# Kernel tuning notes

Hardware: AMD Instinct MI355X
Metric: run time of the kernel (lower is better)

The kernel has to match this reference:

```python
import jax, jax.numpy as jnp
import numpy as np

K_NN = 20  # neighbors per group (k=20 in source)


def fps_one(xyz, npoint):
    # xyz: [N,3] -> indices [npoint] via iterative furthest point sampling
    N = xyz.shape[0]
    def body(carry, _):
        dist, far = carry
        d = jnp.sum((xyz - xyz[far]) ** 2, axis=-1)
        dist = jnp.minimum(dist, d)
        return (dist, jnp.argmax(dist).astype(jnp.int32)), far
    init = (jnp.full((N,), 1e10, xyz.dtype), jnp.int32(0))
    _, idx = jax.lax.scan(body, init, None, length=npoint)
    return idx


def gather(pts, idx):
    # pts: [B,M,C], idx: [B,...] -> [B,...,C]
    return jax.vmap(lambda p, i: p[i])(pts, idx)


def knn(q, ref, k):
    # q: [B,S,3], ref: [B,M,3] -> [B,S,k] indices of nearest refs
    d = (jnp.sum(q * q, -1, keepdims=True)
         - 2.0 * jnp.einsum('bsc,bmc->bsm', q, ref)
         + jnp.sum(ref * ref, -1)[:, None, :])
    _, idx = jax.lax.top_k(-d, k)
    return idx


def sa_block(xyz, feats, npoint, W, b):
    # Set abstraction: FPS sample -> kNN group -> shared MLP -> max pool
    fidx = jax.vmap(fps_one, in_axes=(0, None))(xyz, npoint)   # [B,S]
    new_xyz = gather(xyz, fidx)                                 # [B,S,3]
    nidx = knn(new_xyz, xyz, K_NN)                              # [B,S,K]
    rel = gather(xyz, nidx) - new_xyz[:, :, None, :]            # [B,S,K,3]
    grp = jnp.concatenate([rel, gather(feats, nidx)], -1)       # [B,S,K,3+C]
    h = jax.nn.relu(jnp.einsum('bskc,cd->bskd', grp, W) + b)
    return new_xyz, jnp.max(h, axis=2)                          # [B,S,Cout]


def fp_block(xq, xr, fr, skip, W, b):
    # Feature propagation: 3-NN inverse-distance interp -> concat skip -> MLP
    idx = knn(xq, xr, 3)                                        # [B,S,3]
    d = jnp.sum((gather(xr, idx) - xq[:, :, None, :]) ** 2, -1)
    w = 1.0 / (d + 1e-8)
    w = w / jnp.sum(w, -1, keepdims=True)
    interp = jnp.einsum('bsk,bskc->bsc', w, gather(fr, idx))
    cat = jnp.concatenate([interp, skip], -1)
    return jax.nn.relu(jnp.einsum('bsc,cd->bsd', cat, W) + b)


def setup_inputs() -> dict:
    key = jax.random.key(0)
    ks = jax.random.split(key, 24)
    B, N = 8, 4096
    x = jax.random.normal(ks[0], (B, 6, N), jnp.float32)
    cls_label = jax.random.uniform(ks[1], (B, 16), jnp.float32)
    def lin(k, cin, cout):
        kw, kb = jax.random.split(k)
        s = 1.0 / np.sqrt(cin)
        return (jax.random.normal(kw, (cin, cout), jnp.float32) * s,
                jax.random.normal(kb, (cout,), jnp.float32) * 0.01)
    W0, b0 = lin(ks[2], 6, 64)
    W1, b1 = lin(ks[3], 67, 128)
    W2, b2 = lin(ks[4], 131, 256)
    W3, b3 = lin(ks[5], 259, 512)
    F3, fb3 = lin(ks[6], 768, 512)
    F2, fb2 = lin(ks[7], 640, 256)
    F1, fb1 = lin(ks[8], 320, 128)
    F0, fb0 = lin(ks[9], 150, 128)
    Wseg, bseg = lin(ks[10], 128, 50)
    return {"x": x, "cls_label": cls_label,
            "W0": W0, "b0": b0, "W1": W1, "b1": b1, "W2": W2, "b2": b2,
            "W3": W3, "b3": b3, "F3": F3, "fb3": fb3, "F2": F2, "fb2": fb2,
            "F1": F1, "fb1": fb1, "F0": F0, "fb0": fb0,
            "Wseg": Wseg, "bseg": bseg}


def reference(x, cls_label, W0, b0, W1, b1, W2, b2, W3, b3,
              F3, fb3, F2, fb2, F1, fb1, F0, fb0, Wseg, bseg):
    B, _, N = x.shape
    xyz = jnp.transpose(x[:, :3, :], (0, 2, 1))   # [B,N,3]
    nrm = jnp.transpose(x[:, 3:, :], (0, 2, 1))   # [B,N,3]
    # hierarchical set abstraction (512 -> 256 -> 128 -> 64 points)
    x1, f1 = sa_block(xyz, nrm, 512, W0, b0)      # f1: [B,512,64]
    x2, f2 = sa_block(x1, f1, 256, W1, b1)        # f2: [B,256,128]
    x3, f3 = sa_block(x2, f2, 128, W2, b2)        # f3: [B,128,256]
    x4, f4 = sa_block(x3, f3, 64, W3, b3)         # f4: [B,64,512]
    # feature propagation back up
    g3 = fp_block(x3, x4, f4, f3, F3, fb3)        # [B,128,512]
    g2 = fp_block(x2, x3, g3, f2, F2, fb2)        # [B,256,256]
    g1 = fp_block(x1, x2, g2, f1, F1, fb1)        # [B,512,128]
    cls = jnp.broadcast_to(cls_label[:, None, :], (B, N, 16))
    skip0 = jnp.concatenate([cls, xyz, nrm], -1)  # [B,N,22]
    g0 = fp_block(xyz, x1, g1, skip0, F0, fb0)    # [B,N,128]
    result = jnp.einsum('bnc,cd->bnd', g0, Wseg) + bseg  # [B,N,50]
    return result, jnp.transpose(g0, (0, 2, 1))
```

## Files before the change

### kernel.cpp

```cpp
#include <hip/hip_runtime.h>
#include <float.h>

#define B8 8
#define NPTS 4096

__global__ void split_xyz_kernel(const float* __restrict__ x,
                                 float* __restrict__ xyz, float* __restrict__ nrm,
                                 float4* __restrict__ xyz4) {
#pragma clang fp contract(off)
  int g = blockIdx.x * 256 + threadIdx.x;
  if (g >= B8 * NPTS) return;
  int b = g / NPTS, n = g % NPTS;
  const float* xb = x + (size_t)b * 6 * NPTS;
  float* o1 = xyz + (size_t)g * 3;
  float* o2 = nrm + (size_t)g * 3;
  float a0 = xb[0 * NPTS + n], a1 = xb[1 * NPTS + n], a2 = xb[2 * NPTS + n];
  o1[0] = a0; o1[1] = a1; o1[2] = a2;
  xyz4[g] = make_float4(a0, a1, a2, a0 * a0 + a1 * a1 + a2 * a2);
  o2[0] = xb[3 * NPTS + n]; o2[1] = xb[4 * NPTS + n]; o2[2] = xb[5 * NPTS + n];
}

template <int CTRL, int RM>
__device__ __forceinline__ unsigned dppmov(unsigned v) {
  return (unsigned)__builtin_amdgcn_update_dpp((int)v, (int)v, CTRL, RM, 0xf, false);
}

template <int CTRL, int RM>
__device__ __forceinline__ void red_key_max(unsigned& kh, unsigned& kl) {
  unsigned oh = dppmov<CTRL, RM>(kh);
  unsigned ol = dppmov<CTRL, RM>(kl);
  unsigned long long ko = ((unsigned long long)oh << 32) | ol;
  unsigned long long k  = ((unsigned long long)kh << 32) | kl;
  bool c = ko > k;
  kh = c ? oh : kh;
  kl = c ? ol : kl;
}

template <int CTRL, int RM>
__device__ __forceinline__ void red_key_min(unsigned& kh, unsigned& kl) {
  unsigned oh = dppmov<CTRL, RM>(kh);
  unsigned ol = dppmov<CTRL, RM>(kl);
  unsigned long long ko = ((unsigned long long)oh << 32) | ol;
  unsigned long long k  = ((unsigned long long)kh << 32) | kl;
  bool c = ko < k;
  kh = c ? oh : kh;
  kl = c ? ol : kl;
}

#define WAVE_RED_MAX(kh, kl)            \
  red_key_max<0x111, 0xf>(kh, kl);      \
  red_key_max<0x112, 0xf>(kh, kl);      \
  red_key_max<0x114, 0xf>(kh, kl);      \
  red_key_max<0x118, 0xf>(kh, kl);      \
  red_key_max<0x142, 0xa>(kh, kl);      \
  red_key_max<0x143, 0xc>(kh, kl);

#define WAVE_RED_MIN(kh, kl)            \
  red_key_min<0x111, 0xf>(kh, kl);      \
  red_key_min<0x112, 0xf>(kh, kl);      \
  red_key_min<0x114, 0xf>(kh, kl);      \
  red_key_min<0x118, 0xf>(kh, kl);      \
  red_key_min<0x142, 0xa>(kh, kl);      \
  red_key_min<0x143, 0xc>(kh, kl);

template <int BLOCK, int P>
__global__ __launch_bounds__(BLOCK) void fps4_kernel(const float* __restrict__ xyz,
                                                     int N, int S,
                                                     float* __restrict__ out_xyz) {
#pragma clang fp contract(off)
  constexpr int NW = BLOCK / 64;
  __shared__ float4 pts[BLOCK * P];
  __shared__ float4 sel[512];
  __shared__ alignas(16) unsigned long long wkey[2][NW];
  int b = blockIdx.x, t = threadIdx.x;
  const float* p = xyz + (size_t)b * N * 3;
  float px[P], py[P], pz[P], dist[P];
#pragma unroll
  for (int j = 0; j < P; ++j) {
    int idx = t + j * BLOCK;
    float a = p[3 * idx], bb = p[3 * idx + 1], c = p[3 * idx + 2];
    px[j] = a; py[j] = bb; pz[j] = c;
    pts[idx] = make_float4(a, bb, c, 0.f);
    dist[j] = 1e10f;
  }
  __syncthreads();
  float fx = p[0], fy = p[1], fz = p[2];
  for (int i = 0; i < S; ++i) {
    if (t == 0) sel[i] = make_float4(fx, fy, fz, 0.f);
    float bv = -1.0f;
    int bj = 0;
#pragma unroll
    for (int j = 0; j < P; ++j) {
      float dx = px[j] - fx, dy = py[j] - fy, dz = pz[j] - fz;
      float d = dx * dx + dy * dy + dz * dz;
      float nd = fminf(dist[j], d);
      dist[j] = nd;
      bool c = nd > bv;
      bv = c ? nd : bv;
      bj = c ? j : bj;
    }
    unsigned kh = __float_as_uint(bv);
    unsigned kl = (unsigned)(~(t + bj * BLOCK));
    WAVE_RED_MAX(kh, kl);
    int buf = i & 1;
    if ((t & 63) == 63)
      wkey[buf][t >> 6] = ((unsigned long long)kh << 32) | kl;
    __syncthreads();
    unsigned long long g = 0ull;
    const ulonglong2* wk2 = (const ulonglong2*)&wkey[buf][0];
#pragma unroll
    for (int w = 0; w < NW / 2; ++w) {
      ulonglong2 e = wk2[w];
      unsigned long long m = (e.x > e.y) ? e.x : e.y;
      g = (m > g) ? m : g;
    }
    int far = (int)~(unsigned)g;
    float4 f = pts[far];
    fx = f.x; fy = f.y; fz = f.z;
  }
  __syncthreads();
  for (int i = t; i < S; i += BLOCK) {
    float4 f = sel[i];
    float* o = out_xyz + ((size_t)b * S + i) * 3;
    o[0] = f.x; o[1] = f.y; o[2] = f.z;
  }
}

__global__ __launch_bounds__(64) void knn20_kernel(const float* __restrict__ q,
                                                   const float4* __restrict__ ref4,
                                                   int* __restrict__ nidx) {
#pragma clang fp contract(off)
  int bs = blockIdx.x;
  int b = bs >> 9;
  int t = threadIdx.x;
  __shared__ float sd[4096];
  const float* qp = q + (size_t)bs * 3;
  float qx = qp[0], qy = qp[1], qz = qp[2];
  float qq = qx * qx + qy * qy + qz * qz;
  const float4* rp = ref4 + (size_t)b * 4096;
  float v1 = FLT_MAX, v2 = FLT_MAX;
  int i1 = 0, i2 = 0;
  for (int k = 0; k < 64; ++k) {
    int i = t + (k << 6);
    float4 r = rp[i];
    float dot = qx * r.x + qy * r.y + qz * r.z;
    float d = qq - 2.0f * dot + r.w;
    sd[i] = d;
    if (d < v1) { v2 = v1; i2 = i1; v1 = d; i1 = i; }
    else if (d < v2) { v2 = d; i2 = i; }
  }
  __syncthreads();
  unsigned keep = 0;
  for (int k = 0; k < 20; ++k) {
    unsigned kh = __float_as_uint(v1), kl = (unsigned)i1;
    WAVE_RED_MIN(kh, kl);
    unsigned w = (unsigned)__builtin_amdgcn_readlane((int)kl, 63);
    if (t == k) keep = w;
    if (t == 0) sd[w] = FLT_MAX;
    __syncthreads();
    if (((int)w & 63) == t) {
      v1 = v2; i1 = i2;
      v2 = FLT_MAX; i2 = 0;
      if (v1 == FLT_MAX) {
        for (int kk = 0; kk < 64; ++kk) {
          int i = t + (kk << 6);
          float d = sd[i];
          if (d < v1) { v2 = v1; i2 = i1; v1 = d; i1 = i; }
          else if (d < v2) { v2 = d; i2 = i; }
        }
      }
    }
  }
  if (t < 20) nidx[(size_t)bs * 20 + t] = (int)keep;
}

__global__ __launch_bounds__(256) void sa1_kernel(
    const float* __restrict__ xyz, const float* __restrict__ nrm,
    const float* __restrict__ x1, const int* __restrict__ nidx,
    const float* __restrict__ W, const float* __restrict__ bias,
    float* __restrict__ f1) {
#pragma clang fp contract(off)
  __shared__ alignas(16) float smem_in[4][20][8];
  int wv = threadIdx.x >> 6, t = threadIdx.x & 63;
  int g = blockIdx.x * 4 + wv;
  int b = g >> 9;
  if (t < 20) {
    int id = nidx[(size_t)g * 20 + t];
    const float* xr = xyz + ((size_t)b * 4096 + id) * 3;
    const float* xq = x1 + (size_t)g * 3;
    const float* nr = nrm + ((size_t)b * 4096 + id) * 3;
    smem_in[wv][t][0] = xr[0] - xq[0];
    smem_in[wv][t][1] = xr[1] - xq[1];
    smem_in[wv][t][2] = xr[2] - xq[2];
    smem_in[wv][t][3] = nr[0];
    smem_in[wv][t][4] = nr[1];
    smem_in[wv][t][5] = nr[2];
    smem_in[wv][t][6] = 0.0f;
    smem_in[wv][t][7] = 0.0f;
  }
  __syncthreads();
  float w0 = W[0 * 64 + t], w1 = W[1 * 64 + t], w2 = W[2 * 64 + t];
  float w3 = W[3 * 64 + t], w4 = W[4 * 64 + t], w5 = W[5 * 64 + t];
  float bb = bias[t];
  float m = 0.0f;
  for (int n = 0; n < 20; ++n) {
    const float4 a = *reinterpret_cast<const float4*>(&smem_in[wv][n][0]);
    const float4 c = *reinterpret_cast<const float4*>(&smem_in[wv][n][4]);
    float v = a.x * w0;
    v += a.y * w1;
    v += a.z * w2;
    v += a.w * w3;
    v += c.x * w4;
    v += c.y * w5;
    v += bb;
    m = fmaxf(m, v);
  }
  f1[(size_t)g * 64 + t] = m;
}

__device__ __forceinline__ void knn3_store(int g, const float* rx3,
                                           float qx, float qy, float qz,
                                           int i0, int i1, int i2,
                                           int* __restrict__ idx3,
                                           float* __restrict__ w3) {
#pragma clang fp contract(off)
  int ii[3] = {i0, i1, i2};
  float w[3];
  float wsum = 0.0f;
#pragma unroll
  for (int k = 0; k < 3; ++k) {
    const float* r = rx3 + (size_t)ii[k] * 3;
    float dx = r[0] - qx, dy = r[1] - qy, dz = r[2] - qz;
    float d = dx * dx + dy * dy + dz * dz;
    w[k] = 1.0f / (d + 1e-8f);
    wsum += w[k];
  }
#pragma unroll
  for (int k = 0; k < 3; ++k) {
    idx3[(size_t)g * 3 + k] = ii[k];
    w3[(size_t)g * 3 + k] = w[k] / wsum;
  }
}

__global__ __launch_bounds__(256) void neighbors_kernel(
    const float* __restrict__ xyz, const float* __restrict__ x1,
    int* __restrict__ nidx2, int* __restrict__ nidx3, int* __restrict__ nidx4,
    int* __restrict__ idx3_3, float* __restrict__ w3_3,
    int* __restrict__ idx3_2, float* __restrict__ w3_2,
    int* __restrict__ idx3_1, float* __restrict__ w3_1,
    int* __restrict__ idx3_0, float* __restrict__ w3_0) {
#pragma clang fp contract(off)
  __shared__ float4 smem4[512];
  int blk = blockIdx.x, tid = threadIdx.x;

  if (blk < 896) {
    int S, M, qid;
    int* nout;
    const int wv = tid >> 6, t64 = tid & 63;
    if (blk < 512)      { S = 256; M = 512; qid = blk * 4 + wv;         nout = nidx2; }
    else if (blk < 768) { S = 128; M = 256; qid = (blk - 512) * 4 + wv; nout = nidx3; }
    else                { S = 64;  M = 128; qid = (blk - 768) * 4 + wv; nout = nidx4; }
    float* swd = (float*)smem4 + wv * M;
    int b = qid / S, s = qid % S;
    const float* qp = x1 + ((size_t)b * 512 + s) * 3;
    float qx = qp[0], qy = qp[1], qz = qp[2];
    float qq = qx * qx + qy * qy + qz * qz;
    const float* rp = x1 + (size_t)b * 512 * 3;
    for (int i = t64; i < M; i += 64) {
      float rx = rp[3 * i], ry = rp[3 * i + 1], rz = rp[3 * i + 2];
      float rr = rx * rx + ry * ry + rz * rz;
      float dot = qx * rx + qy * ry + qz * rz;
      swd[i] = qq - 2.0f * dot + rr;
    }
    __syncthreads();
    unsigned keep = 0;
    for (int k = 0; k < 20; ++k) {
      float bv = FLT_MAX;
      int bi = 0;
      for (int i = t64; i < M; i += 64) {
        float v = swd[i];
        bool c = v < bv;
        bv = c ? v : bv;
        bi = c ? i : bi;
      }
      unsigned kh = __float_as_uint(bv), kl = (unsigned)bi;
      WAVE_RED_MIN(kh, kl);
      unsigned w = (unsigned)__builtin_amdgcn_readlane((int)kl, 63);
      if (t64 == k) keep = w;
      if (t64 == 0) swd[w] = FLT_MAX;
      __syncthreads();
    }
    if (t64 < 20) nout[(size_t)qid * 20 + t64] = (int)keep;
    return;
  }

  if (blk < 900) {
    int g = (blk - 896) * 256 + tid;
    int Sq = 128, M = 64;
    int b = g / Sq, s = g % Sq;
    const float* qp = x1 + ((size_t)b * 512 + s) * 3;
    float qx = qp[0], qy = qp[1], qz = qp[2];
    float qq = qx * qx + qy * qy + qz * qz;
    const float* rp = x1 + (size_t)b * 512 * 3;
    float v0 = FLT_MAX, v1 = FLT_MAX, v2 = FLT_MAX;
    int i0 = 0, i1 = 0, i2 = 0;
    for (int i = 0; i < M; ++i) {
      float rx = rp[3 * i], ry = rp[3 * i + 1], rz = rp[3 * i + 2];
      float d = qq - 2.0f * (qx * rx + qy * ry + qz * rz) + (rx * rx + ry * ry + rz * rz);
      if (d < v2) {
        if (d < v1) {
          if (d < v0) { v2 = v1; i2 = i1; v1 = v0; i1 = i0; v0 = d; i0 = i; }
          else { v2 = v1; i2 = i1; v1 = d; i1 = i; }
        } else { v2 = d; i2 = i; }
      }
    }
    knn3_store(g, rp, qx, qy, qz, i0, i1, i2, idx3_3, w3_3);
    return;
  }

  int g, Sq, M, LDQ;
  int* oidx;
  float* ow;
  const float* q;
  if (blk < 908)      { g = (blk - 900) * 256 + tid; Sq = 256;  M = 128; oidx = idx3_2; ow = w3_2; q = x1;  LDQ = 512; }
  else if (blk < 924) { g = (blk - 908) * 256 + tid; Sq = 512;  M = 256; oidx = idx3_1; ow = w3_1; q = x1;  LDQ = 512; }
  else                { g = (blk - 924) * 256 + tid; Sq = 4096; M = 512; oidx = idx3_0; ow = w3_0; q = xyz; LDQ = 4096; }
  int b = g / Sq, s = g % Sq;
  const float* rp = x1 + (size_t)b * 512 * 3;
  for (int i = tid; i < M; i += 256) {
    float rx = rp[3 * i], ry = rp[3 * i + 1], rz = rp[3 * i + 2];
    smem4[i] = make_float4(rx, ry, rz, rx * rx + ry * ry + rz * rz);
  }
  __syncthreads();
  const float* qp = q + ((size_t)b * LDQ + s) * 3;
  float qx = qp[0], qy = qp[1], qz = qp[2];
  float qq = qx * qx + qy * qy + qz * qz;
  float v0 = FLT_MAX, v1 = FLT_MAX, v2 = FLT_MAX;
  int i0 = 0, i1 = 0, i2 = 0;
  for (int i = 0; i < M; ++i) {
    float4 r = smem4[i];
    float d = qq - 2.0f * (qx * r.x + qy * r.y + qz * r.z) + r.w;
    if (d < v2) {
      if (d < v1) {
        if (d < v0) { v2 = v1; i2 = i1; v1 = v0; i1 = i0; v0 = d; i0 = i; }
        else { v2 = v1; i2 = i1; v1 = d; i1 = i; }
      } else { v2 = d; i2 = i; }
    }
  }
  {
    int ii[3] = {i0, i1, i2};
    float w[3];
    float wsum = 0.0f;
#pragma unroll
    for (int k = 0; k < 3; ++k) {
      float4 r = smem4[ii[k]];
      float dx = r.x - qx, dy = r.y - qy, dz = r.z - qz;
      float d = dx * dx + dy * dy + dz * dz;
      w[k] = 1.0f / (d + 1e-8f);
      wsum += w[k];
    }
#pragma unroll
    for (int k = 0; k < 3; ++k) {
      oidx[(size_t)g * 3 + k] = ii[k];
      ow[(size_t)g * 3 + k] = w[k] / wsum;
    }
  }
}

#define GEMM_STAGE(k0v, ...)                                                      \
    {                                                                             \
      int r_ = (int)threadIdx.x & 63;                                             \
      int ks_ = (int)threadIdx.x >> 6;                                            \
      int rr = rowBase + r_;                                                      \
      int kq0 = (k0v) + ks_ * 4;                                                  \
      float4 va = make_float4(0.f, 0.f, 0.f, 0.f);                                \
      if (rr < Mrows) { __VA_ARGS__ }                                             \
      areg4 = va;                                                                 \
    }                                                                             \
    {                                                                             \
      int kk = (int)threadIdx.x >> 4;                                             \
      int n4 = ((int)threadIdx.x & 15) * 4;                                       \
      int kq = (k0v) + kk, cc = colBase + n4;                                     \
      if (colBase + 64 <= N) {                                                    \
        if (kq < K) breg4 = *reinterpret_cast<const float4*>(&Wm[(size_t)kq * N + cc]); \
        else breg4 = make_float4(0.f, 0.f, 0.f, 0.f);                             \
      } else {                                                                    \
        breg4.x = (kq < K && cc < N) ? Wm[(size_t)kq * N + cc] : 0.0f;            \
        breg4.y = (kq < K && cc + 1 < N) ? Wm[(size_t)kq * N + cc + 1] : 0.0f;    \
        breg4.z = (kq < K && cc + 2 < N) ? Wm[(size_t)kq * N + cc + 2] : 0.0f;    \
        breg4.w = (kq < K && cc + 3 < N) ? Wm[(size_t)kq * N + cc + 3] : 0.0f;    \
      }                                                                           \
    }

#define GEMM_WRITE_LDS(bufv)                                                      \
    {                                                                             \
      int r_ = (int)threadIdx.x & 63;                                             \
      int k4_ = ((int)threadIdx.x >> 6) * 4;                                      \
      As[bufv][k4_ + 0][r_] = areg4.x;                                            \
      As[bufv][k4_ + 1][r_] = areg4.y;                                            \
      As[bufv][k4_ + 2][r_] = areg4.z;                                            \
      As[bufv][k4_ + 3][r_] = areg4.w;                                            \
    }                                                                             \
    *reinterpret_cast<float4*>(&Bs[bufv][threadIdx.x >> 4][(threadIdx.x & 15) * 4]) = breg4;

#define GEMM_MAIN(...)                                                            \
  __shared__ alignas(16) float As[2][16][68];                                     \
  __shared__ alignas(16) float Bs[2][16][64];                                     \
  int tx = threadIdx.x & 15, ty = threadIdx.x >> 4;                               \
  int rowBase = blockIdx.y * 64;                                                  \
  int colBase = blockIdx.x * 64;                                                  \
  float acc[4][4] = {};                                                           \
  float4 areg4, breg4;                                                            \
  GEMM_STAGE(kLo, __VA_ARGS__)                                                    \
  GEMM_WRITE_LDS(0)                                                               \
  __syncthreads();                                                                \
  int cur = 0;                                                                    \
  for (int k0 = kLo; k0 < kHi; k0 += 16) {                                        \
    int nxt = cur ^ 1;                                                            \
    bool more = (k0 + 16 < kHi);                                                  \
    if (more) { GEMM_STAGE(k0 + 16, __VA_ARGS__) }                                \
    _Pragma("unroll")                                                             \
    for (int kk = 0; kk < 16; ++kk) {                                             \
      const float4 av = *reinterpret_cast<const float4*>(&As[cur][kk][ty * 4]);   \
      const float4 bv = *reinterpret_cast<const float4*>(&Bs[cur][kk][tx * 4]);   \
      acc[0][0] += av.x * bv.x; acc[0][1] += av.x * bv.y;                         \
      acc[0][2] += av.x * bv.z; acc[0][3] += av.x * bv.w;                         \
      acc[1][0] += av.y * bv.x; acc[1][1] += av.y * bv.y;                         \
      acc[1][2] += av.y * bv.z; acc[1][3] += av.y * bv.w;                         \
      acc[2][0] += av.z * bv.x; acc[2][1] += av.z * bv.y;                         \
      acc[2][2] += av.z * bv.z; acc[2][3] += av.z * bv.w;                         \
      acc[3][0] += av.w * bv.x; acc[3][1] += av.w * bv.y;                         \
      acc[3][2] += av.w * bv.z; acc[3][3] += av.w * bv.w;                         \
    }                                                                             \
    if (more) { GEMM_WRITE_LDS(nxt) }                                             \
    __syncthreads();                                                              \
    cur = nxt;                                                                    \
  }

#define GEMM_EPI_STORE                                                            \
  _Pragma("unroll")                                                               \
  for (int i = 0; i < 4; ++i) {                                                   \
    int row = rowBase + ty * 4 + i;                                               \
    if (row >= Mrows) continue;                                                   \
    _Pragma("unroll")                                                             \
    for (int j = 0; j < 4; ++j) {                                                 \
      int col = colBase + tx * 4 + j;                                             \
      if (col >= N) continue;                                                     \
      float v = acc[i][j] + bias[col];                                            \
      if (RELU) v = fmaxf(v, 0.0f);                                               \
      C[(size_t)row * N + col] = v;                                               \
    }                                                                             \
  }

__global__ __launch_bounds__(256) void gemm_kernel(const float* __restrict__ A,
                                                   const float* __restrict__ Wm,
                                                   const float* __restrict__ bias,
                                                   float* __restrict__ C,
                                                   int Mrows, int N, int K, int RELU) {
  const int kLo = 0, kHi = K;
  GEMM_MAIN(
    if (kq0 + 3 < K) {
      va = *reinterpret_cast<const float4*>(&A[(size_t)rr * K + kq0]);
    } else {
      va.x = (kq0 < K) ? A[(size_t)rr * K + kq0] : 0.0f;
      va.y = (kq0 + 1 < K) ? A[(size_t)rr * K + kq0 + 1] : 0.0f;
      va.z = (kq0 + 2 < K) ? A[(size_t)rr * K + kq0 + 2] : 0.0f;
      va.w = (kq0 + 3 < K) ? A[(size_t)rr * K + kq0 + 3] : 0.0f;
    }
  )
  GEMM_EPI_STORE
}

__global__ __launch_bounds__(256) void gemm_sa_kernel(
    const float* __restrict__ xyz, const float* __restrict__ feats,
    const float* __restrict__ new_xyz, const int* __restrict__ nidx,
    const float* __restrict__ Wm, const float* __restrict__ bias,
    float* __restrict__ fOut, int Mref, int LDR, int S, int LDQ, int Cf,
    int Mrows, int N, int K) {
  const int kLo = 0, kHi = K;
  GEMM_MAIN(
    int bs = rr / 20;
    int s_ = bs % S;
    int b = bs / S;
    int id = nidx[rr];
    const float* xr_ = xyz + ((size_t)b * LDR + id) * 3;
    const float* xq_ = new_xyz + ((size_t)b * LDQ + s_) * 3;
    const float* fb_ = feats + ((size_t)b * Mref + id) * Cf;
    float* vp_ = (float*)&va;
    _Pragma("unroll")
    for (int c_ = 0; c_ < 4; ++c_) {
      int kq = kq0 + c_;
      float v = 0.0f;
      if (kq < K) v = (kq < 3) ? (xr_[kq] - xq_[kq]) : fb_[kq - 3];
      vp_[c_] = v;
    }
  )
  __shared__ int smax[4][64];
  int gBase = rowBase / 20;
  int nG = (rowBase + 63) / 20 - gBase + 1;
  for (int l = threadIdx.x; l < nG * 64; l += 256) smax[l >> 6][l & 63] = 0;
  __syncthreads();
  {
    int gl = (rowBase + ty * 4) / 20 - gBase;
#pragma unroll
    for (int j = 0; j < 4; ++j) {
      int col = colBase + tx * 4 + j;
      if (col >= N) continue;
      float bb = bias[col];
      float m = 0.0f;
#pragma unroll
      for (int i = 0; i < 4; ++i) {
        int row = rowBase + ty * 4 + i;
        if (row >= Mrows) continue;
        m = fmaxf(m, fmaxf(acc[i][j] + bb, 0.0f));
      }
      atomicMax(&smax[gl][tx * 4 + j], __float_as_int(m));
    }
  }
  __syncthreads();
  for (int l = threadIdx.x; l < nG * 64; l += 256) {
    int g = gBase + (l >> 6), c = colBase + (l & 63);
    if (c < N) atomicMax((int*)&fOut[(size_t)g * N + c], smax[l >> 6][l & 63]);
  }
}

__global__ __launch_bounds__(256) void gemm_fp_kernel(
    const float* __restrict__ fr, const int* __restrict__ idx3,
    const float* __restrict__ w3, const float* __restrict__ skip,
    const float* __restrict__ cls, const float* __restrict__ xyzq,
    const float* __restrict__ nrmq, const float* __restrict__ frBias,
    const float* __restrict__ Wm, const float* __restrict__ bias,
    float* __restrict__ C, int Sq, int Mr, int Cr, int Cs, int mode,
    int SPLITK, int CHUNK,
    int Mrows, int N, int K) {
  const int kLo = blockIdx.z * CHUNK;
  const int kHi = min(K, kLo + CHUNK);
  GEMM_MAIN(
    int bs = rr;
    int b = bs / Sq;
    const int* ii_ = idx3 + (size_t)bs * 3;
    const float* ww_ = w3 + (size_t)bs * 3;
    int i0_ = ii_[0], i1_ = ii_[1], i2_ = ii_[2];
    float w0_ = ww_[0], w1_ = ww_[1], w2_ = ww_[2];
    const float* fb_ = fr + (size_t)b * Mr * Cr;
    float* vp_ = (float*)&va;
    _Pragma("unroll")
    for (int c_ = 0; c_ < 4; ++c_) {
      int kq = kq0 + c_;
      float v = 0.0f;
      if (kq < K) {
        if (kq < Cr) {
          float a0 = fb_[(size_t)i0_ * Cr + kq];
          float a1 = fb_[(size_t)i1_ * Cr + kq];
          float a2 = fb_[(size_t)i2_ * Cr + kq];
          if (frBias) {
            float bb = frBias[kq];
            a0 = fmaxf(a0 + bb, 0.0f);
            a1 = fmaxf(a1 + bb, 0.0f);
            a2 = fmaxf(a2 + bb, 0.0f);
          }
          v = w0_ * a0;
          v += w1_ * a1;
          v += w2_ * a2;
        } else {
          int cc = kq - Cr;
          if (mode == 0) {
            v = skip[(size_t)bs * Cs + cc];
          } else {
            if (cc < 16) v = cls[(size_t)b * 16 + cc];
            else if (cc < 19) v = xyzq[(size_t)bs * 3 + (cc - 16)];
            else v = nrmq[(size_t)bs * 3 + (cc - 19)];
          }
        }
      }
      vp_[c_] = v;
    }
  )
  if (SPLITK) {
#pragma unroll
    for (int i = 0; i < 4; ++i) {
      int row = rowBase + ty * 4 + i;
      if (row >= Mrows) continue;
#pragma unroll
      for (int j = 0; j < 4; ++j) {
        int col = colBase + tx * 4 + j;
        if (col >= N) continue;
        atomicAdd(&C[(size_t)row * N + col], acc[i][j]);
      }
    }
  } else {
    const int RELU = 1;
    GEMM_EPI_STORE
  }
}

__global__ __launch_bounds__(256) void transpose_g0_kernel(const float* __restrict__ g0,
                                                           float* __restrict__ out2) {
  __shared__ float tile[32][33];
  int n0 = blockIdx.x * 32, c0 = blockIdx.y * 32, b = blockIdx.z;
  int tx = threadIdx.x & 31, ty = threadIdx.x >> 5;
#pragma unroll
  for (int j = 0; j < 32; j += 8)
    tile[ty + j][tx] = g0[((size_t)b * NPTS + n0 + ty + j) * 128 + c0 + tx];
  __syncthreads();
#pragma unroll
  for (int j = 0; j < 32; j += 8)
    out2[((size_t)b * 128 + c0 + ty + j) * NPTS + n0 + tx] = tile[tx][ty + j];
}

static inline int cdiv(int a, int b) { return (a + b - 1) / b; }

extern "C" void kernel_launch(void* const* d_in, const int* in_sizes, int n_in,
                              void* d_out, int out_size, void* d_ws, size_t ws_size,
                              hipStream_t stream) {
  const float* x    = (const float*)d_in[0];
  const float* cls  = (const float*)d_in[1];
  const float* W0 = (const float*)d_in[2];  const float* b0 = (const float*)d_in[3];
  const float* W1 = (const float*)d_in[4];  const float* b1 = (const float*)d_in[5];
  const float* W2 = (const float*)d_in[6];  const float* b2 = (const float*)d_in[7];
  const float* W3 = (const float*)d_in[8];  const float* b3 = (const float*)d_in[9];
  const float* F3 = (const float*)d_in[10]; const float* fb3 = (const float*)d_in[11];
  const float* F2 = (const float*)d_in[12]; const float* fb2 = (const float*)d_in[13];
  const float* F1 = (const float*)d_in[14]; const float* fb1 = (const float*)d_in[15];
  const float* F0 = (const float*)d_in[16]; const float* fb0 = (const float*)d_in[17];
  const float* Wseg = (const float*)d_in[18]; const float* bseg = (const float*)d_in[19];
  float* out = (float*)d_out;

  float* ws = (float*)d_ws;
  size_t off = 0;
  auto alloc = [&](size_t n) { float* p = ws + off; off += (n + 3) & ~(size_t)3; return p; };
  float* xyz = alloc(8 * 4096 * 3);
  float* nrm = alloc(8 * 4096 * 3);
  float4* xyz4 = (float4*)alloc(8 * 4096 * 4);
  float* x1 = alloc(8 * 512 * 3);
  float* f1 = alloc(8 * 512 * 64);
  float* f2 = alloc(8 * 256 * 128);
  float* f3 = alloc(8 * 128 * 256);
  float* f4 = alloc(8 * 64 * 512);
  float* g3 = alloc(8 * 128 * 512);
  float* g2 = alloc(8 * 256 * 256);
  float* g1 = alloc(8 * 512 * 128);
  float* g0 = alloc(8 * 4096 * 128);
  int* nidx1 = (int*)alloc(8 * 512 * 20);
  int* nidx2 = (int*)alloc(8 * 256 * 20);
  int* nidx3 = (int*)alloc(8 * 128 * 20);
  int* nidx4 = (int*)alloc(8 * 64 * 20);
  int* idx3_3 = (int*)alloc(8 * 128 * 3);  float* w3_3 = alloc(8 * 128 * 3);
  int* idx3_2 = (int*)alloc(8 * 256 * 3);  float* w3_2 = alloc(8 * 256 * 3);
  int* idx3_1 = (int*)alloc(8 * 512 * 3);  float* w3_1 = alloc(8 * 512 * 3);
  int* idx3_0 = (int*)alloc(8 * 4096 * 3); float* w3_0 = alloc(8 * 4096 * 3);

  hipMemsetAsync(f1, 0,
                 ((size_t)8 * (512 * 64 + 256 * 128 + 128 * 256 + 64 * 512) +
                  (size_t)8 * (128 * 512 + 256 * 256 + 512 * 128)) * 4, stream);

  split_xyz_kernel<<<cdiv(8 * 4096, 256), 256, 0, stream>>>(x, xyz, nrm, xyz4);
  fps4_kernel<256, 16><<<8, 256, 0, stream>>>(xyz, 4096, 512, x1);
  knn20_kernel<<<8 * 512, 64, 0, stream>>>(x1, xyz4, nidx1);
  sa1_kernel<<<1024, 256, 0, stream>>>(xyz, nrm, x1, nidx1, W0, b0, f1);
  neighbors_kernel<<<1052, 256, 0, stream>>>(xyz, x1, nidx2, nidx3, nidx4,
                                             idx3_3, w3_3, idx3_2, w3_2,
                                             idx3_1, w3_1, idx3_0, w3_0);

  {
    dim3 grid(2, cdiv(8 * 256 * 20, 64));
    gemm_sa_kernel<<<grid, 256, 0, stream>>>(x1, f1, x1, nidx2, W1, b1, f2,
                                             512, 512, 256, 512, 64,
                                             8 * 256 * 20, 128, 67);
  }
  {
    dim3 grid(4, cdiv(8 * 128 * 20, 64));
    gemm_sa_kernel<<<grid, 256, 0, stream>>>(x1, f2, x1, nidx3, W2, b2, f3,
                                             256, 512, 128, 512, 128,
                                             8 * 128 * 20, 256, 131);
  }
  {
    dim3 grid(8, cdiv(8 * 64 * 20, 64));
    gemm_sa_kernel<<<grid, 256, 0, stream>>>(x1, f3, x1, nidx4, W3, b3, f4,
                                             128, 512, 64, 512, 256,
                                             8 * 64 * 20, 512, 259);
  }

  {
    dim3 grid(8, cdiv(8 * 128, 64), 4);
    gemm_fp_kernel<<<grid, 256, 0, stream>>>(f4, idx3_3, w3_3, f3, nullptr, nullptr, nullptr,
                                             nullptr, F3, fb3, g3, 128, 64, 512, 256, 0,
                                             1, 192, 8 * 128, 512, 768);
  }
  {
    dim3 grid(4, cdiv(8 * 256, 64), 4);
    gemm_fp_kernel<<<grid, 256, 0, stream>>>(g3, idx3_2, w3_2, f2, nullptr, nullptr, nullptr,
                                             fb3, F2, fb2, g2, 256, 128, 512, 128, 0,
                                             1, 160, 8 * 256, 256, 640);
  }
  {
    dim3 grid(2, cdiv(8 * 512, 64), 2);
    gemm_fp_kernel<<<grid, 256, 0, stream>>>(g2, idx3_1, w3_1, f1, nullptr, nullptr, nullptr,
                                             fb2, F1, fb1, g1, 512, 256, 256, 64, 0,
                                             1, 160, 8 * 512, 128, 320);
  }
  {
    dim3 grid(2, cdiv(8 * 4096, 64), 1);
    gemm_fp_kernel<<<grid, 256, 0, stream>>>(g1, idx3_0, w3_0, nullptr, cls, xyz, nrm,
                                             fb1, F0, fb0, g0, 4096, 512, 128, 22, 1,
                                             0, 160, 8 * 4096, 128, 150);
  }

  {
    dim3 grid(1, cdiv(8 * 4096, 64));
    gemm_kernel<<<grid, 256, 0, stream>>>(g0, Wseg, bseg, out, 8 * 4096, 50, 128, 0);
  }
  transpose_g0_kernel<<<dim3(128, 4, 8), 256, 0, stream>>>(g0, out + (size_t)8 * 4096 * 50);
}
```

Baseline: 960.9 us.

## Fuse input split into FPS, SA1 MLP into kNN, and g0 transpose into seg GEMM

```diff
diff --git a/kernel.cpp b/kernel.cpp
--- a/kernel.cpp
+++ b/kernel.cpp
@@ -3,22 +3,6 @@
 
 #define B8 8
 #define NPTS 4096
-
-__global__ void split_xyz_kernel(const float* __restrict__ x,
-                                 float* __restrict__ xyz, float* __restrict__ nrm,
-                                 float4* __restrict__ xyz4) {
-#pragma clang fp contract(off)
-  int g = blockIdx.x * 256 + threadIdx.x;
-  if (g >= B8 * NPTS) return;
-  int b = g / NPTS, n = g % NPTS;
-  const float* xb = x + (size_t)b * 6 * NPTS;
-  float* o1 = xyz + (size_t)g * 3;
-  float* o2 = nrm + (size_t)g * 3;
-  float a0 = xb[0 * NPTS + n], a1 = xb[1 * NPTS + n], a2 = xb[2 * NPTS + n];
-  o1[0] = a0; o1[1] = a1; o1[2] = a2;
-  xyz4[g] = make_float4(a0, a1, a2, a0 * a0 + a1 * a1 + a2 * a2);
-  o2[0] = xb[3 * NPTS + n]; o2[1] = xb[4 * NPTS + n]; o2[2] = xb[5 * NPTS + n];
-}
 
 template <int CTRL, int RM>
 __device__ __forceinline__ unsigned dppmov(unsigned v) {
@@ -64,7 +48,10 @@
   red_key_min<0x143, 0xc>(kh, kl);
 
 template <int BLOCK, int P>
-__global__ __launch_bounds__(BLOCK) void fps4_kernel(const float* __restrict__ xyz,
+__global__ __launch_bounds__(BLOCK) void fps4_kernel(const float* __restrict__ x,
+                                                     float* __restrict__ xyz,
+                                                     float* __restrict__ nrm,
+                                                     float4* __restrict__ xyz4,
                                                      int N, int S,
                                                      float* __restrict__ out_xyz) {
 #pragma clang fp contract(off)
@@ -73,18 +60,25 @@
   __shared__ float4 sel[512];
   __shared__ alignas(16) unsigned long long wkey[2][NW];
   int b = blockIdx.x, t = threadIdx.x;
-  const float* p = xyz + (size_t)b * N * 3;
+  const float* xb = x + (size_t)b * 6 * N;
   float px[P], py[P], pz[P], dist[P];
 #pragma unroll
   for (int j = 0; j < P; ++j) {
     int idx = t + j * BLOCK;
-    float a = p[3 * idx], bb = p[3 * idx + 1], c = p[3 * idx + 2];
+    float a = xb[0 * N + idx], bb = xb[1 * N + idx], c = xb[2 * N + idx];
     px[j] = a; py[j] = bb; pz[j] = c;
     pts[idx] = make_float4(a, bb, c, 0.f);
     dist[j] = 1e10f;
+    size_t g = (size_t)b * N + idx;
+    float* o1 = xyz + g * 3;
+    o1[0] = a; o1[1] = bb; o1[2] = c;
+    xyz4[g] = make_float4(a, bb, c, a * a + bb * bb + c * c);
+    float n0 = xb[3 * N + idx], n1 = xb[4 * N + idx], n2 = xb[5 * N + idx];
+    float* o2 = nrm + g * 3;
+    o2[0] = n0; o2[1] = n1; o2[2] = n2;
   }
   __syncthreads();
-  float fx = p[0], fy = p[1], fz = p[2];
+  float fx = xb[0], fy = xb[N], fz = xb[2 * N];
   for (int i = 0; i < S; ++i) {
     if (t == 0) sel[i] = make_float4(fx, fy, fz, 0.f);
     float bv = -1.0f;
@@ -128,12 +122,16 @@
 
 __global__ __launch_bounds__(64) void knn20_kernel(const float* __restrict__ q,
                                                    const float4* __restrict__ ref4,
-                                                   int* __restrict__ nidx) {
+                                                   const float* __restrict__ nrm,
+                                                   const float* __restrict__ W,
+                                                   const float* __restrict__ bias,
+                                                   float* __restrict__ f1) {
 #pragma clang fp contract(off)
   int bs = blockIdx.x;
   int b = bs >> 9;
   int t = threadIdx.x;
   __shared__ float sd[4096];
+  __shared__ alignas(16) float smem_in[20][8];
   const float* qp = q + (size_t)bs * 3;
   float qx = qp[0], qy = qp[1], qz = qp[2];
   float qq = qx * qx + qy * qy + qz * qz;
@@ -171,32 +169,18 @@
       }
     }
   }
-  if (t < 20) nidx[(size_t)bs * 20 + t] = (int)keep;
-}
-
-__global__ __launch_bounds__(256) void sa1_kernel(
-    const float* __restrict__ xyz, const float* __restrict__ nrm,
-    const float* __restrict__ x1, const int* __restrict__ nidx,
-    const float* __restrict__ W, const float* __restrict__ bias,
-    float* __restrict__ f1) {
-#pragma clang fp contract(off)
-  __shared__ alignas(16) float smem_in[4][20][8];
-  int wv = threadIdx.x >> 6, t = threadIdx.x & 63;
-  int g = blockIdx.x * 4 + wv;
-  int b = g >> 9;
   if (t < 20) {
-    int id = nidx[(size_t)g * 20 + t];
-    const float* xr = xyz + ((size_t)b * 4096 + id) * 3;
-    const float* xq = x1 + (size_t)g * 3;
+    int id = (int)keep;
+    float4 r = rp[id];
     const float* nr = nrm + ((size_t)b * 4096 + id) * 3;
-    smem_in[wv][t][0] = xr[0] - xq[0];
-    smem_in[wv][t][1] = xr[1] - xq[1];
-    smem_in[wv][t][2] = xr[2] - xq[2];
-    smem_in[wv][t][3] = nr[0];
-    smem_in[wv][t][4] = nr[1];
-    smem_in[wv][t][5] = nr[2];
-    smem_in[wv][t][6] = 0.0f;
-    smem_in[wv][t][7] = 0.0f;
+    smem_in[t][0] = r.x - qx;
+    smem_in[t][1] = r.y - qy;
+    smem_in[t][2] = r.z - qz;
+    smem_in[t][3] = nr[0];
+    smem_in[t][4] = nr[1];
+    smem_in[t][5] = nr[2];
+    smem_in[t][6] = 0.0f;
+    smem_in[t][7] = 0.0f;
   }
   __syncthreads();
   float w0 = W[0 * 64 + t], w1 = W[1 * 64 + t], w2 = W[2 * 64 + t];
@@ -204,8 +188,8 @@
   float bb = bias[t];
   float m = 0.0f;
   for (int n = 0; n < 20; ++n) {
-    const float4 a = *reinterpret_cast<const float4*>(&smem_in[wv][n][0]);
-    const float4 c = *reinterpret_cast<const float4*>(&smem_in[wv][n][4]);
+    const float4 a = *reinterpret_cast<const float4*>(&smem_in[n][0]);
+    const float4 c = *reinterpret_cast<const float4*>(&smem_in[n][4]);
     float v = a.x * w0;
     v += a.y * w1;
     v += a.z * w2;
@@ -215,7 +199,7 @@
     v += bb;
     m = fmaxf(m, v);
   }
-  f1[(size_t)g * 64 + t] = m;
+  f1[(size_t)bs * 64 + t] = m;
 }
 
 __device__ __forceinline__ void knn3_store(int g, const float* rx3,
@@ -452,20 +436,20 @@
     }                                                                             \
   }
 
-__global__ __launch_bounds__(256) void gemm_kernel(const float* __restrict__ A,
-                                                   const float* __restrict__ Wm,
-                                                   const float* __restrict__ bias,
-                                                   float* __restrict__ C,
-                                                   int Mrows, int N, int K, int RELU) {
+__global__ __launch_bounds__(256) void gemm_seg_kernel(const float* __restrict__ A,
+                                                       const float* __restrict__ Wm,
+                                                       const float* __restrict__ bias,
+                                                       float* __restrict__ C,
+                                                       float* __restrict__ T,
+                                                       int Mrows, int N, int K) {
   const int kLo = 0, kHi = K;
+  const int RELU = 0;
   GEMM_MAIN(
-    if (kq0 + 3 < K) {
-      va = *reinterpret_cast<const float4*>(&A[(size_t)rr * K + kq0]);
-    } else {
-      va.x = (kq0 < K) ? A[(size_t)rr * K + kq0] : 0.0f;
-      va.y = (kq0 + 1 < K) ? A[(size_t)rr * K + kq0 + 1] : 0.0f;
-      va.z = (kq0 + 2 < K) ? A[(size_t)rr * K + kq0 + 2] : 0.0f;
-      va.w = (kq0 + 3 < K) ? A[(size_t)rr * K + kq0 + 3] : 0.0f;
+    va = *reinterpret_cast<const float4*>(&A[(size_t)rr * K + kq0]);
+    {
+      int n_ = rr & 4095, b_ = rr >> 12;
+      float* tp = T + (((size_t)b_ * 128 + kq0) * 4096 + n_);
+      tp[0] = va.x; tp[4096] = va.y; tp[8192] = va.z; tp[12288] = va.w;
     }
   )
   GEMM_EPI_STORE
@@ -594,20 +578,6 @@
   }
 }
 
-__global__ __launch_bounds__(256) void transpose_g0_kernel(const float* __restrict__ g0,
-                                                           float* __restrict__ out2) {
-  __shared__ float tile[32][33];
-  int n0 = blockIdx.x * 32, c0 = blockIdx.y * 32, b = blockIdx.z;
-  int tx = threadIdx.x & 31, ty = threadIdx.x >> 5;
-#pragma unroll
-  for (int j = 0; j < 32; j += 8)
-    tile[ty + j][tx] = g0[((size_t)b * NPTS + n0 + ty + j) * 128 + c0 + tx];
-  __syncthreads();
-#pragma unroll
-  for (int j = 0; j < 32; j += 8)
-    out2[((size_t)b * 128 + c0 + ty + j) * NPTS + n0 + tx] = tile[tx][ty + j];
-}
-
 static inline int cdiv(int a, int b) { return (a + b - 1) / b; }
 
 extern "C" void kernel_launch(void* const* d_in, const int* in_sizes, int n_in,
@@ -641,7 +611,6 @@
   float* g2 = alloc(8 * 256 * 256);
   float* g1 = alloc(8 * 512 * 128);
   float* g0 = alloc(8 * 4096 * 128);
-  int* nidx1 = (int*)alloc(8 * 512 * 20);
   int* nidx2 = (int*)alloc(8 * 256 * 20);
   int* nidx3 = (int*)alloc(8 * 128 * 20);
   int* nidx4 = (int*)alloc(8 * 64 * 20);
@@ -654,10 +623,8 @@
                  ((size_t)8 * (512 * 64 + 256 * 128 + 128 * 256 + 64 * 512) +
                   (size_t)8 * (128 * 512 + 256 * 256 + 512 * 128)) * 4, stream);
 
-  split_xyz_kernel<<<cdiv(8 * 4096, 256), 256, 0, stream>>>(x, xyz, nrm, xyz4);
-  fps4_kernel<256, 16><<<8, 256, 0, stream>>>(xyz, 4096, 512, x1);
-  knn20_kernel<<<8 * 512, 64, 0, stream>>>(x1, xyz4, nidx1);
-  sa1_kernel<<<1024, 256, 0, stream>>>(xyz, nrm, x1, nidx1, W0, b0, f1);
+  fps4_kernel<256, 16><<<8, 256, 0, stream>>>(x, xyz, nrm, xyz4, 4096, 512, x1);
+  knn20_kernel<<<8 * 512, 64, 0, stream>>>(x1, xyz4, nrm, W0, b0, f1);
   neighbors_kernel<<<1052, 256, 0, stream>>>(xyz, x1, nidx2, nidx3, nidx4,
                                              idx3_3, w3_3, idx3_2, w3_2,
                                              idx3_1, w3_1, idx3_0, w3_0);
@@ -708,7 +675,8 @@
 
   {
     dim3 grid(1, cdiv(8 * 4096, 64));
-    gemm_kernel<<<grid, 256, 0, stream>>>(g0, Wseg, bseg, out, 8 * 4096, 50, 128, 0);
-  }
-  transpose_g0_kernel<<<dim3(128, 4, 8), 256, 0, stream>>>(g0, out + (size_t)8 * 4096 * 50);
-}
+    gemm_seg_kernel<<<grid, 256, 0, stream>>>(g0, Wseg, bseg, out,
+                                              out + (size_t)8 * 4096 * 50,
+                                              8 * 4096, 50, 128);
+  }
+}
```

After: 956.5 us. About the same (-0.5%).
